# Optimization experiments

Measured on AMD Instinct MI355X. Metric: run time of the kernel, lower is better.

Reference implementation:

```python
import jax, jax.numpy as jnp
import numpy as np

N = 16      # hparams.length (utterances)
T = 128     # tokens per utterance
D = 256     # local_feature_dim
DG = 256    # global_attention.input_dim
ATT = 128   # attention inner dim
R1 = 2 * N * N  # rgcn num_relations
H1 = 256    # rgcn.dim
H2 = 256    # gcn.dim
NEG = -1e9


def setup_inputs() -> dict:
    ks = jax.random.split(jax.random.key(0), 16)
    s = 0.02
    return {
        "global_features": jax.random.normal(ks[0], (N, DG), jnp.float32),
        "local_features": jax.random.normal(ks[1], (N, T, D), jnp.float32),
        "speaker": jax.random.randint(ks[2], (N,), 0, 2),
        "length": jax.random.randint(ks[3], (N,), 1, T + 1),
        # Bahdanau global attention params
        "Wq": jax.random.normal(ks[4], (DG, ATT), jnp.float32) * s,
        "Wk": jax.random.normal(ks[5], (DG, ATT), jnp.float32) * s,
        "v_att": jax.random.normal(ks[6], (ATT,), jnp.float32) * s,
        # Bidirectional local attention params
        "Wb1": jax.random.normal(ks[7], (D, ATT), jnp.float32) * s,
        "Wb2": jax.random.normal(ks[8], (D, ATT), jnp.float32) * s,
        # RGCN layer 1 (2*N^2 relations)
        "Wrel1": jax.random.normal(ks[9], (R1, D, H1), jnp.float32) * s,
        "Wroot1": jax.random.normal(ks[10], (D, H1), jnp.float32) * s,
        "b1": jnp.zeros((H1,), jnp.float32),
        # RGCN layer 2 (1 relation)
        "Wrel2": jax.random.normal(ks[11], (1, H1, H2), jnp.float32) * s,
        "Wroot2": jax.random.normal(ks[12], (H1, H2), jnp.float32) * s,
        "b2": jnp.zeros((H2,), jnp.float32),
    }


def _rgcn_fg(x, Wrel, Wroot, b, e_src, e_dst, rel, ew, n_nodes):
    # x: [N,T,din], ew: [E,Ts,Td] (src-token x dst-token weights), Wrel: [R,din,dout]
    We = Wrel[rel]                 # [E,din,dout] irregular gather over relations
    xs = x[e_src]                  # [E,T,din]
    # message aligned with dst tokens: sum over src tokens t -> dst token s
    msg = jnp.einsum('ets,etd,edo->eso', ew, xs, We)   # [E,T,dout]
    agg = jax.ops.segment_sum(msg, e_dst, num_segments=n_nodes)
    return agg + x @ Wroot + b


def reference(global_features, local_features, speaker, length,
              Wq, Wk, v_att, Wb1, Wb2,
              Wrel1, Wroot1, b1, Wrel2, Wroot2, b2):
    n = global_features.shape[0]
    t = local_features.shape[1]

    # --- Bahdanau global attention: query i over keys j ---
    q = global_features @ Wq                         # [N,A]
    k = global_features @ Wk                         # [N,A]
    s = jnp.tanh(q[:, None, :] + k[None, :, :]) @ v_att   # [N,N]
    gw = jax.nn.softmax(s, axis=1).reshape(-1)       # [N*N]

    # --- Bidirectional local attention, vectorized over all (i,j) pairs ---
    p1 = local_features @ Wb1                        # [N,T,A]
    p2 = local_features @ Wb2                        # [N,T,A]
    S = jnp.einsum('ita,jsa->ijts', p1, p2)          # [N,N,T,T]
    pos = jnp.arange(t)
    valid = pos[None, :] < length[:, None]           # [N,T]
    S = jnp.where(valid[None, :, None, :], S, NEG)   # mask key tokens of j
    w1 = jax.nn.softmax(S, axis=-1)                  # softmax over j's tokens
    w1 = w1 * valid[:, None, :, None]                # zero padded query rows of i
    lw = w1.reshape(n * n, t, t)                     # [E,T,T]

    # --- edge weights & relation ids ---
    ew1 = gw[:, None, None] * lw                     # [E,T,T]
    e_src = jnp.arange(n * n) // n                   # edge (i,j): src=i
    e_dst = jnp.arange(n * n) % n                    # dst=j
    direction = jnp.where(e_src < e_dst, 0, 1)
    rel = (speaker[e_src] * n + speaker[e_dst]) * 2 + direction

    # --- two attention-weighted relational GCN layers ---
    x1 = _rgcn_fg(local_features, Wrel1, Wroot1, b1, e_src, e_dst, rel, ew1, n)
    x2 = _rgcn_fg(x1, Wrel2, Wroot2, b2, e_src, e_dst, jnp.zeros_like(rel), lw, n)
    return x2
```

## Files before the change

### kernel.cpp

```cpp
#include <hip/hip_runtime.h>

#define NODES 16
#define TT    128
#define DIM   256
#define ATTD  128
#define HD    256
#define NEGV  -1e9f

typedef short bf16x8 __attribute__((ext_vector_type(8)));
typedef float f32x4  __attribute__((ext_vector_type(4)));
typedef unsigned short ushort_t;
typedef ushort_t u16x4 __attribute__((ext_vector_type(4)));
typedef ushort_t u16x8 __attribute__((ext_vector_type(8)));

__device__ __forceinline__ ushort_t f2b(float f) {
  union { float f; unsigned u; } v; v.f = f;
  unsigned r = (v.u + 0x7fffu + ((v.u >> 16) & 1u)) >> 16;
  return (ushort_t)r;
}

__device__ __forceinline__ void wave_gemm_step(const ushort_t* __restrict__ A, int as, int R0,
                                               const ushort_t* __restrict__ BT, int bs, int C0,
                                               int kb, int lr, f32x4 acc[4][4]) {
  bf16x8 a[4], b[4];
#pragma unroll
  for (int m = 0; m < 4; ++m)
    a[m] = *(const bf16x8*)(A + (size_t)(R0 + m * 16 + lr) * as + kb);
#pragma unroll
  for (int n = 0; n < 4; ++n)
    b[n] = *(const bf16x8*)(BT + (size_t)(C0 + n * 16 + lr) * bs + kb);
#pragma unroll
  for (int m = 0; m < 4; ++m)
#pragma unroll
    for (int n = 0; n < 4; ++n)
      acc[m][n] = __builtin_amdgcn_mfma_f32_16x16x32_bf16(a[m], b[n], acc[m][n], 0, 0, 0);
}

#define WAVE_SETUP                                    \
  int tid = threadIdx.x;                              \
  int wave = tid >> 6, lane = tid & 63;               \
  int wr = wave >> 1, wc = wave & 1;                  \
  int lr = lane & 15, kg = lane >> 4;                 \
  (void)wr; (void)wc;

#define ACC_INIT(acc)                                 \
  f32x4 acc[4][4];                                    \
  { f32x4 z = {0.f, 0.f, 0.f, 0.f};                   \
    _Pragma("unroll") for (int m = 0; m < 4; ++m)     \
    _Pragma("unroll") for (int n = 0; n < 4; ++n) acc[m][n] = z; }

__device__ __forceinline__ void stage_tile(const ushort_t* __restrict__ src,
                                           ushort_t* __restrict__ dst, int tid) {
#pragma unroll
  for (int p = 0; p < 8; ++p) {
    int idx = p * 256 + tid;
    int row = idx >> 4;
    int cb  = (idx & 15) << 4;
    u16x8 v = *(const u16x8*)(src + (size_t)row * 128 + (cb >> 1));
    *(u16x8*)((char*)dst + row * 256 + (cb ^ ((row & 7) << 4))) = v;
  }
}

__device__ __forceinline__ void lds_gemm128(const ushort_t* __restrict__ A,
                                            const ushort_t* __restrict__ B,
                                            int R0, int C0, int lr, int kg,
                                            f32x4 acc[4][4]) {
#pragma unroll
  for (int kk = 0; kk < 4; ++kk) {
    int cb = kk * 64 + kg * 16;
    bf16x8 a[4], b[4];
#pragma unroll
    for (int m = 0; m < 4; ++m) {
      int row = R0 + m * 16 + lr;
      a[m] = *(const bf16x8*)((const char*)A + row * 256 + (cb ^ ((row & 7) << 4)));
    }
#pragma unroll
    for (int n = 0; n < 4; ++n) {
      int row = C0 + n * 16 + lr;
      b[n] = *(const bf16x8*)((const char*)B + row * 256 + (cb ^ ((row & 7) << 4)));
    }
#pragma unroll
    for (int m = 0; m < 4; ++m)
#pragma unroll
      for (int n = 0; n < 4; ++n)
        acc[m][n] = __builtin_amdgcn_mfma_f32_16x16x32_bf16(a[m], b[n], acc[m][n], 0, 0, 0);
  }
}

__global__ void k_prep(const float* __restrict__ Lf, ushort_t* __restrict__ Lfh,
                       const float* __restrict__ Wb1, const float* __restrict__ Wb2,
                       const float* __restrict__ Wroot1, const float* __restrict__ Wroot2,
                       const float* __restrict__ Wrel2, const float* __restrict__ Wrel1,
                       ushort_t* __restrict__ Wb1T, ushort_t* __restrict__ Wb2T,
                       ushort_t* __restrict__ Wroot1T, ushort_t* __restrict__ Wroot2T,
                       ushort_t* __restrict__ Wrel2T, ushort_t* __restrict__ Wrel1T8,
                       const float* __restrict__ G, const float* __restrict__ Wq,
                       const float* __restrict__ Wk, float* __restrict__ qk) {
  int blk = blockIdx.x;
  if (blk < 256) {
    int gi = blk * 256 + threadIdx.x;
    const float4* src = (const float4*)Lf;
    float4 v0 = src[gi * 2], v1 = src[gi * 2 + 1];
    u16x8 o;
    o[0] = f2b(v0.x); o[1] = f2b(v0.y); o[2] = f2b(v0.z); o[3] = f2b(v0.w);
    o[4] = f2b(v1.x); o[5] = f2b(v1.y); o[6] = f2b(v1.z); o[7] = f2b(v1.w);
    *(u16x8*)(Lfh + (size_t)gi * 8) = o;
  } else if (blk < 448) {
    __shared__ float lds[64][65];
    int b = blk - 256;
    const float* src; ushort_t* dst; int R, C, t;
    if (b < 8)       { src = Wb1;    dst = Wb1T;    R = 256; C = 128; t = b; }
    else if (b < 16) { src = Wb2;    dst = Wb2T;    R = 256; C = 128; t = b - 8; }
    else if (b < 32) { src = Wroot1; dst = Wroot1T; R = 256; C = 256; t = b - 16; }
    else if (b < 48) { src = Wroot2; dst = Wroot2T; R = 256; C = 256; t = b - 32; }
    else if (b < 64) { src = Wrel2;  dst = Wrel2T;  R = 256; C = 256; t = b - 48; }
    else {
      int m = (b - 64) >> 4;
      int relid = (m >> 2) * 32 + (m & 3);
      src = Wrel1 + (size_t)relid * 65536;
      dst = Wrel1T8 + (size_t)m * 65536;
      R = 256; C = 256; t = (b - 64) & 15;
    }
    int tilesC = C >> 6;
    int r0 = (t / tilesC) * 64, c0 = (t % tilesC) * 64;
    int tid = threadIdx.x;
    for (int p = 0; p < 16; ++p) {
      int idx = p * 256 + tid, rr = idx >> 6, cc = idx & 63;
      lds[rr][cc] = src[(size_t)(r0 + rr) * C + c0 + cc];
    }
    __syncthreads();
    for (int p = 0; p < 16; ++p) {
      int idx = p * 256 + tid, rr = idx >> 6, cc = idx & 63;
      dst[(size_t)(c0 + rr) * R + r0 + cc] = f2b(lds[cc][rr]);
    }
  } else {
    int i = blk - 448, t = threadIdx.x;
    const float* W = (t < 128) ? Wq : Wk;
    int a = t & 127;
    float acc = 0.f;
#pragma unroll 8
    for (int d = 0; d < DIM; ++d)
      acc = fmaf(G[i * DIM + d], W[d * ATTD + a], acc);
    int dst = (t < 128) ? i : (NODES + i);
    qk[(size_t)dst * ATTD + a] = acc;
  }
}

__global__ __launch_bounds__(256, 1)
void k_phaseB(const float* __restrict__ qk, const float* __restrict__ vatt,
              float* __restrict__ gw,
              const ushort_t* __restrict__ Lfh,
              const ushort_t* __restrict__ Wb1T, const ushort_t* __restrict__ Wb2T,
              ushort_t* __restrict__ p1h, ushort_t* __restrict__ p2h,
              const ushort_t* __restrict__ Wroot1T, const float* __restrict__ b1,
              float* __restrict__ x1part,
              const ushort_t* __restrict__ Wrel1T8, const int* __restrict__ spk,
              ushort_t* __restrict__ YT) {
  int blk = blockIdx.x;
  if (blk < 16) {
    __shared__ float sred[NODES][17];
    __shared__ float q[ATTD];
    int i = blk, t = threadIdx.x;
    int j = t >> 4, ag = t & 15;
    if (t < ATTD) q[t] = qk[(size_t)i * ATTD + t];
    __syncthreads();
    float sum = 0.f;
#pragma unroll
    for (int u = 0; u < 8; ++u) {
      int a = ag * 8 + u;
      sum += tanhf(q[a] + qk[(size_t)(NODES + j) * ATTD + a]) * vatt[a];
    }
    sred[j][ag] = sum;
    __syncthreads();
    if (t < NODES) {
      float s = 0.f;
#pragma unroll
      for (int u = 0; u < 16; ++u) s += sred[t][u];
      sred[t][16] = s;
    }
    __syncthreads();
    if (t == 0) {
      float m = -1e30f;
      for (int jj = 0; jj < NODES; ++jj) m = fmaxf(m, sred[jj][16]);
      float ex[NODES], ssum = 0.f;
      for (int jj = 0; jj < NODES; ++jj) { ex[jj] = __expf(sred[jj][16] - m); ssum += ex[jj]; }
      float inv = 1.f / ssum;
      for (int jj = 0; jj < NODES; ++jj) gw[i * NODES + jj] = ex[jj] * inv;
    }
  } else if (blk < 48) {
    int t = blk - 16;
    int sel = t >> 4, bx = t & 15;
    const ushort_t* BT = sel ? Wb2T : Wb1T;
    ushort_t* out = sel ? p2h : p1h;
    WAVE_SETUP
    int R0 = bx * 128 + wr * 64, C0 = wc * 64;
    ACC_INIT(acc)
    for (int kk = 0; kk < 8; ++kk)
      wave_gemm_step(Lfh, DIM, R0, BT, DIM, C0, kk * 32 + kg * 8, lr, acc);
#pragma unroll
    for (int m = 0; m < 4; ++m)
#pragma unroll
      for (int n = 0; n < 4; ++n) {
        int col = C0 + n * 16 + lr;
#pragma unroll
        for (int r = 0; r < 4; ++r) {
          int row = R0 + m * 16 + kg * 4 + r;
          out[(size_t)row * ATTD + col] = f2b(acc[m][n][r]);
        }
      }
  } else if (blk < 80) {
    int t = blk - 48;
    int bx = t & 15, by = t >> 4;
    WAVE_SETUP
    int R0 = bx * 128 + wr * 64, C0 = by * 128 + wc * 64;
    ACC_INIT(acc)
    for (int kk = 0; kk < 8; ++kk)
      wave_gemm_step(Lfh, DIM, R0, Wroot1T, DIM, C0, kk * 32 + kg * 8, lr, acc);
#pragma unroll
    for (int m = 0; m < 4; ++m)
#pragma unroll
      for (int n = 0; n < 4; ++n) {
        int col = C0 + n * 16 + lr;
        float bb = b1[col];
#pragma unroll
        for (int r = 0; r < 4; ++r) {
          int row = R0 + m * 16 + kg * 4 + r;
          x1part[(size_t)row * HD + col] = acc[m][n][r] + bb;
        }
      }
  } else {
    int t = blk - 80;
    int iq = t >> 1, cy = t & 1;
    int i = iq >> 2, q = iq & 3;
    int m8 = spk[i] * 4 + q;
    const ushort_t* A  = Lfh + (size_t)i * TT * DIM;
    const ushort_t* BT = Wrel1T8 + (size_t)m8 * 65536;
    WAVE_SETUP
    int R0 = wr * 64, C0 = cy * 128 + wc * 64;
    ACC_INIT(acc)
    for (int kk = 0; kk < 8; ++kk)
      wave_gemm_step(A, DIM, R0, BT, DIM, C0, kk * 32 + kg * 8, lr, acc);
#pragma unroll
    for (int m = 0; m < 4; ++m)
#pragma unroll
      for (int n = 0; n < 4; ++n) {
        int o = C0 + n * 16 + lr;
        int t0 = R0 + m * 16 + kg * 4;
        u16x4 v;
#pragma unroll
        for (int r = 0; r < 4; ++r) v[r] = f2b(acc[m][n][r]);
        *(u16x4*)(YT + (size_t)iq * 32768 + (size_t)o * TT + t0) = v;
      }
  }
}

__global__ __launch_bounds__(256, 1)
void k_locatt(const ushort_t* __restrict__ p1h, const ushort_t* __restrict__ p2h,
              const int* __restrict__ length,
              ushort_t* __restrict__ lwT) {
  __shared__ float S[TT][129];
  __shared__ float red[TT][2];
  __shared__ float sInv[TT];
  int e = blockIdx.x, i = e >> 4, j = e & 15;
  WAVE_SETUP
  int R0 = wr * 64, C0 = wc * 64;
  const ushort_t* A = p1h + (size_t)i * TT * ATTD;
  const ushort_t* B = p2h + (size_t)j * TT * ATTD;
  ACC_INIT(acc)
  for (int kk = 0; kk < 4; ++kk)
    wave_gemm_step(A, ATTD, R0, B, ATTD, C0, kk * 32 + kg * 8, lr, acc);
#pragma unroll
  for (int m = 0; m < 4; ++m)
#pragma unroll
    for (int n = 0; n < 4; ++n)
#pragma unroll
      for (int r = 0; r < 4; ++r)
        S[R0 + m * 16 + kg * 4 + r][C0 + n * 16 + lr] = acc[m][n][r];
  __syncthreads();
  int leni = length[i], lenj = length[j];
  int t = tid & 127, h = tid >> 7, s0 = h * 64;
  float mx = -1e30f;
  for (int s = s0; s < s0 + 64; ++s) {
    float vv = (s < lenj) ? S[t][s] : NEGV;
    mx = fmaxf(mx, vv);
  }
  red[t][h] = mx;
  __syncthreads();
  mx = fmaxf(red[t][0], red[t][1]);
  __syncthreads();
  float sum = 0.f;
  for (int s = s0; s < s0 + 64; ++s) {
    float vv = (s < lenj) ? S[t][s] : NEGV;
    float ee = __expf(vv - mx);
    S[t][s] = ee;
    sum += ee;
  }
  red[t][h] = sum;
  __syncthreads();
  if (h == 0) sInv[t] = (t < leni) ? 1.f / (red[t][0] + red[t][1]) : 0.f;
  __syncthreads();
  int s = tid >> 1;
  int t0 = (tid & 1) * 64;
  size_t base = (size_t)e * 16384 + (size_t)s * TT;
  for (int tb = 0; tb < 64; tb += 8) {
    u16x8 w;
#pragma unroll
    for (int u = 0; u < 8; ++u) {
      int tt = t0 + tb + u;
      w[u] = f2b(S[tt][s] * sInv[tt]);
    }
    *(u16x8*)(lwT + base + t0 + tb) = w;
  }
}

__global__ __launch_bounds__(256, 1)
void k_wagg(const ushort_t* __restrict__ lwT, const ushort_t* __restrict__ Bsrc,
            const float* __restrict__ gw, const int* __restrict__ spk,
            float* __restrict__ part, int mode) {
  __shared__ ushort_t lds[4][16384];
  int g = blockIdx.x, j = blockIdx.y, oh = blockIdx.z;
  WAVE_SETUP
  int R0 = wr * 64, C0 = wc * 64;
  int i0 = g * 2, i1 = g * 2 + 1;
  int e0 = i0 * NODES + j, e1 = i1 * NODES + j;
  const ushort_t* B0;
  const ushort_t* B1;
  float ge0, ge1;
  if (mode == 1) {
    int q0 = spk[j] * 2 + ((i0 < j) ? 0 : 1);
    int q1 = spk[j] * 2 + ((i1 < j) ? 0 : 1);
    B0 = Bsrc + (size_t)(i0 * 4 + q0) * 32768 + (size_t)oh * 16384;
    B1 = Bsrc + (size_t)(i1 * 4 + q1) * 32768 + (size_t)oh * 16384;
    ge0 = gw[e0]; ge1 = gw[e1];
  } else {
    B0 = Bsrc + (size_t)i0 * 32768 + (size_t)oh * 16384;
    B1 = Bsrc + (size_t)i1 * 32768 + (size_t)oh * 16384;
    ge0 = 1.f; ge1 = 1.f;
  }
  stage_tile(lwT + (size_t)e0 * 16384, lds[0], tid);
  stage_tile(B0, lds[1], tid);
  __syncthreads();
  stage_tile(lwT + (size_t)e1 * 16384, lds[2], tid);
  stage_tile(B1, lds[3], tid);
  ACC_INIT(acc0)
  lds_gemm128(lds[0], lds[1], R0, C0, lr, kg, acc0);
  __syncthreads();
  ACC_INIT(acc1)
  lds_gemm128(lds[2], lds[3], R0, C0, lr, kg, acc1);
  size_t base = (size_t)(g * NODES + j) * TT * HD + (size_t)oh * 128;
#pragma unroll
  for (int m = 0; m < 4; ++m)
#pragma unroll
    for (int n = 0; n < 4; ++n) {
      int ocol = C0 + n * 16 + lr;
#pragma unroll
      for (int r = 0; r < 4; ++r) {
        int s = R0 + m * 16 + kg * 4 + r;
        part[base + (size_t)s * HD + ocol] = ge0 * acc0[m][n][r] + ge1 * acc1[m][n][r];
      }
    }
}

__global__ __launch_bounds__(256, 1)
void k_reduce1(const float* __restrict__ part, const float* __restrict__ x1part,
               ushort_t* __restrict__ x1h, ushort_t* __restrict__ x1T) {
  __shared__ ushort_t L[TT][136];
  int j = blockIdx.x, oh = blockIdx.y, tid = threadIdx.x;
  const size_t Q = (size_t)NODES * TT * HD;
  for (int p = 0; p < 16; ++p) {
    int idx = p * 256 + tid;
    int t = idx >> 5, o4 = (idx & 31) * 4;
    size_t goff = ((size_t)j * TT + t) * HD + (size_t)oh * 128 + o4;
    float4 s = *(const float4*)(x1part + goff);
    for (int g = 0; g < 8; ++g) {
      float4 pv = *(const float4*)(part + (size_t)g * Q + goff);
      s.x += pv.x; s.y += pv.y; s.z += pv.z; s.w += pv.w;
    }
    u16x4 hv; hv[0] = f2b(s.x); hv[1] = f2b(s.y); hv[2] = f2b(s.z); hv[3] = f2b(s.w);
    *(u16x4*)(x1h + goff) = hv;
    *(u16x4*)(&L[t][o4]) = hv;
  }
  __syncthreads();
  for (int p = 0; p < 16; ++p) {
    int idx = p * 256 + tid;
    int o = idx >> 5, t4 = (idx & 31) * 4;
    u16x4 v;
#pragma unroll
    for (int u = 0; u < 4; ++u) v[u] = L[t4 + u][o];
    *(u16x4*)(x1T + (size_t)j * 32768 + (size_t)(oh * 128 + o) * TT + t4) = v;
  }
}

__global__ void k_reduce2(const float* __restrict__ part, ushort_t* __restrict__ Z2h) {
  int idx = blockIdx.x * 256 + threadIdx.x;
  size_t o4 = (size_t)idx * 4;
  const size_t Q = (size_t)NODES * TT * HD;
  float4 s = *(const float4*)(part + o4);
  for (int g = 1; g < 8; ++g) {
    float4 pv = *(const float4*)(part + (size_t)g * Q + o4);
    s.x += pv.x; s.y += pv.y; s.z += pv.z; s.w += pv.w;
  }
  u16x4 hv; hv[0] = f2b(s.x); hv[1] = f2b(s.y); hv[2] = f2b(s.z); hv[3] = f2b(s.w);
  *(u16x4*)(Z2h + o4) = hv;
}

__global__ __launch_bounds__(64, 1)
void k_final(const ushort_t* __restrict__ Z2h, const ushort_t* __restrict__ Wrel2T,
             const ushort_t* __restrict__ x1h, const ushort_t* __restrict__ Wroot2T,
             const float* __restrict__ b2, float* __restrict__ out) {
  int lane = threadIdx.x;
  int lr = lane & 15, kg = lane >> 4;
  int R0 = blockIdx.x * 64, C0 = blockIdx.y * 64;
  ACC_INIT(acc)
  for (int kk = 0; kk < 8; ++kk)
    wave_gemm_step(Z2h, HD, R0, Wrel2T, HD, C0, kk * 32 + kg * 8, lr, acc);
  for (int kk = 0; kk < 8; ++kk)
    wave_gemm_step(x1h, HD, R0, Wroot2T, HD, C0, kk * 32 + kg * 8, lr, acc);
#pragma unroll
  for (int m = 0; m < 4; ++m)
#pragma unroll
    for (int n = 0; n < 4; ++n) {
      int col = C0 + n * 16 + lr;
      float bb = b2[col];
#pragma unroll
      for (int r = 0; r < 4; ++r) {
        int row = R0 + m * 16 + kg * 4 + r;
        out[(size_t)row * HD + col] = acc[m][n][r] + bb;
      }
    }
}

extern "C" void kernel_launch(void* const* d_in, const int* in_sizes, int n_in,
                              void* d_out, int out_size, void* d_ws, size_t ws_size,
                              hipStream_t stream) {
  (void)in_sizes; (void)n_in; (void)out_size; (void)ws_size;
  const float* G      = (const float*)d_in[0];
  const float* Lf     = (const float*)d_in[1];
  const int*   spk    = (const int*)d_in[2];
  const int*   len    = (const int*)d_in[3];
  const float* Wq     = (const float*)d_in[4];
  const float* Wk     = (const float*)d_in[5];
  const float* vatt   = (const float*)d_in[6];
  const float* Wb1    = (const float*)d_in[7];
  const float* Wb2    = (const float*)d_in[8];
  const float* Wrel1  = (const float*)d_in[9];
  const float* Wroot1 = (const float*)d_in[10];
  const float* b1     = (const float*)d_in[11];
  const float* Wrel2  = (const float*)d_in[12];
  const float* Wroot2 = (const float*)d_in[13];
  const float* b2     = (const float*)d_in[14];

  char* ws = (char*)d_ws;
  const size_t MB = 1ull << 20;
  float*    gw      = (float*)(ws);
  float*    qk      = (float*)(ws + 16 * 1024);
  ushort_t* Lfh     = (ushort_t*)(ws + 1 * MB);
  ushort_t* Wb1T    = (ushort_t*)(ws + 2 * MB);
  ushort_t* Wb2T    = (ushort_t*)(ws + 2 * MB + 64 * 1024);
  ushort_t* Wroot1T = (ushort_t*)(ws + 2 * MB + 128 * 1024);
  ushort_t* Wroot2T = (ushort_t*)(ws + 2 * MB + 256 * 1024);
  ushort_t* Wrel2T  = (ushort_t*)(ws + 2 * MB + 384 * 1024);
  ushort_t* Wrel1T8 = (ushort_t*)(ws + 2 * MB + 512 * 1024);
  ushort_t* p1h     = (ushort_t*)(ws + 4 * MB);
  ushort_t* p2h     = (ushort_t*)(ws + 4 * MB + 512 * 1024);
  ushort_t* lwT     = (ushort_t*)(ws + 5 * MB);
  ushort_t* YT      = (ushort_t*)(ws + 21 * MB);
  float*    x1part  = (float*)(ws + 25 * MB);
  float*    part    = (float*)(ws + 27 * MB);
  ushort_t* x1h     = (ushort_t*)(ws + 43 * MB);
  ushort_t* x1T     = (ushort_t*)(ws + 44 * MB);
  ushort_t* Z2h     = (ushort_t*)(ws + 45 * MB);
  float* out = (float*)d_out;

  k_prep<<<464, 256, 0, stream>>>(Lf, Lfh, Wb1, Wb2, Wroot1, Wroot2, Wrel2, Wrel1,
                                  Wb1T, Wb2T, Wroot1T, Wroot2T, Wrel2T, Wrel1T8,
                                  G, Wq, Wk, qk);
  k_phaseB<<<208, 256, 0, stream>>>(qk, vatt, gw, Lfh, Wb1T, Wb2T, p1h, p2h,
                                    Wroot1T, b1, x1part, Wrel1T8, spk, YT);
  k_locatt<<<256, 256, 0, stream>>>(p1h, p2h, len, lwT);
  k_wagg<<<dim3(8, 16, 2), 256, 0, stream>>>(lwT, YT, gw, spk, part, 1);
  k_reduce1<<<dim3(16, 2), 256, 0, stream>>>(part, x1part, x1h, x1T);
  k_wagg<<<dim3(8, 16, 2), 256, 0, stream>>>(lwT, x1T, gw, spk, part, 2);
  k_reduce2<<<512, 256, 0, stream>>>(part, Z2h);
  k_final<<<dim3(32, 4), 64, 0, stream>>>(Z2h, Wrel2T, x1h, Wroot2T, b2, out);
}
```

Baseline: 91.29 us.

## Stage GEMM operands through swizzled LDS and widen reduce1 grid

Generalizes the LDS tile staging and GEMM helpers to a templated row width. The phase-B projection GEMMs and the local-attention score GEMM now stage A and B tiles into XOR-swizzled shared memory instead of loading MFMA fragments straight from global memory. Separately, k_reduce1 is split into 32-column slices across 128 blocks instead of 32, which adds parallelism to the partial-sum reduction and transpose. The cost is a large static LDS allocation in k_phaseB (128 KB) and k_locatt, which may limit occupancy. Every staging pass also waits on a barrier before any compute starts.

```diff
diff --git a/kernel.cpp b/kernel.cpp
--- a/kernel.cpp
+++ b/kernel.cpp
@@ -49,35 +49,39 @@
     _Pragma("unroll") for (int m = 0; m < 4; ++m)     \
     _Pragma("unroll") for (int n = 0; n < 4; ++n) acc[m][n] = z; }
 
-__device__ __forceinline__ void stage_tile(const ushort_t* __restrict__ src,
-                                           ushort_t* __restrict__ dst, int tid) {
-#pragma unroll
-  for (int p = 0; p < 8; ++p) {
+template <int ROWB>
+__device__ __forceinline__ void stage_tileN(const ushort_t* __restrict__ src,
+                                            ushort_t* __restrict__ dst, int tid) {
+  constexpr int CPR = ROWB / 16;
+  constexpr int PASSES = 128 * CPR / 256;
+#pragma unroll
+  for (int p = 0; p < PASSES; ++p) {
     int idx = p * 256 + tid;
-    int row = idx >> 4;
-    int cb  = (idx & 15) << 4;
-    u16x8 v = *(const u16x8*)(src + (size_t)row * 128 + (cb >> 1));
-    *(u16x8*)((char*)dst + row * 256 + (cb ^ ((row & 7) << 4))) = v;
-  }
-}
-
-__device__ __forceinline__ void lds_gemm128(const ushort_t* __restrict__ A,
-                                            const ushort_t* __restrict__ B,
-                                            int R0, int C0, int lr, int kg,
-                                            f32x4 acc[4][4]) {
-#pragma unroll
-  for (int kk = 0; kk < 4; ++kk) {
+    int row = idx / CPR;
+    int cb  = (idx % CPR) << 4;
+    u16x8 v = *(const u16x8*)(src + (size_t)row * (ROWB / 2) + (cb >> 1));
+    *(u16x8*)((char*)dst + row * ROWB + (cb ^ ((row & 7) << 4))) = v;
+  }
+}
+
+template <int ROWB>
+__device__ __forceinline__ void lds_gemmN(const ushort_t* __restrict__ A,
+                                          const ushort_t* __restrict__ B,
+                                          int R0, int C0, int lr, int kg,
+                                          f32x4 acc[4][4]) {
+#pragma unroll
+  for (int kk = 0; kk < ROWB / 64; ++kk) {
     int cb = kk * 64 + kg * 16;
     bf16x8 a[4], b[4];
 #pragma unroll
     for (int m = 0; m < 4; ++m) {
       int row = R0 + m * 16 + lr;
-      a[m] = *(const bf16x8*)((const char*)A + row * 256 + (cb ^ ((row & 7) << 4)));
+      a[m] = *(const bf16x8*)((const char*)A + row * ROWB + (cb ^ ((row & 7) << 4)));
     }
 #pragma unroll
     for (int n = 0; n < 4; ++n) {
       int row = C0 + n * 16 + lr;
-      b[n] = *(const bf16x8*)((const char*)B + row * 256 + (cb ^ ((row & 7) << 4)));
+      b[n] = *(const bf16x8*)((const char*)B + row * ROWB + (cb ^ ((row & 7) << 4)));
     }
 #pragma unroll
     for (int m = 0; m < 4; ++m)
@@ -156,6 +160,8 @@
               float* __restrict__ x1part,
               const ushort_t* __restrict__ Wrel1T8, const int* __restrict__ spk,
               ushort_t* __restrict__ YT) {
+  __shared__ ushort_t sA[32768];
+  __shared__ ushort_t sB[32768];
   int blk = blockIdx.x;
   if (blk < 16) {
     __shared__ float sred[NODES][17];
@@ -193,10 +199,12 @@
     const ushort_t* BT = sel ? Wb2T : Wb1T;
     ushort_t* out = sel ? p2h : p1h;
     WAVE_SETUP
+    stage_tileN<512>(Lfh + (size_t)bx * 128 * DIM, sA, tid);
+    stage_tileN<512>(BT, sB, tid);
+    __syncthreads();
+    ACC_INIT(acc)
+    lds_gemmN<512>(sA, sB, wr * 64, wc * 64, lr, kg, acc);
     int R0 = bx * 128 + wr * 64, C0 = wc * 64;
-    ACC_INIT(acc)
-    for (int kk = 0; kk < 8; ++kk)
-      wave_gemm_step(Lfh, DIM, R0, BT, DIM, C0, kk * 32 + kg * 8, lr, acc);
 #pragma unroll
     for (int m = 0; m < 4; ++m)
 #pragma unroll
@@ -212,10 +220,12 @@
     int t = blk - 48;
     int bx = t & 15, by = t >> 4;
     WAVE_SETUP
+    stage_tileN<512>(Lfh + (size_t)bx * 128 * DIM, sA, tid);
+    stage_tileN<512>(Wroot1T + (size_t)by * 128 * DIM, sB, tid);
+    __syncthreads();
+    ACC_INIT(acc)
+    lds_gemmN<512>(sA, sB, wr * 64, wc * 64, lr, kg, acc);
     int R0 = bx * 128 + wr * 64, C0 = by * 128 + wc * 64;
-    ACC_INIT(acc)
-    for (int kk = 0; kk < 8; ++kk)
-      wave_gemm_step(Lfh, DIM, R0, Wroot1T, DIM, C0, kk * 32 + kg * 8, lr, acc);
 #pragma unroll
     for (int m = 0; m < 4; ++m)
 #pragma unroll
@@ -233,13 +243,13 @@
     int iq = t >> 1, cy = t & 1;
     int i = iq >> 2, q = iq & 3;
     int m8 = spk[i] * 4 + q;
-    const ushort_t* A  = Lfh + (size_t)i * TT * DIM;
-    const ushort_t* BT = Wrel1T8 + (size_t)m8 * 65536;
     WAVE_SETUP
+    stage_tileN<512>(Lfh + (size_t)i * TT * DIM, sA, tid);
+    stage_tileN<512>(Wrel1T8 + (size_t)m8 * 65536 + (size_t)cy * 128 * DIM, sB, tid);
+    __syncthreads();
+    ACC_INIT(acc)
+    lds_gemmN<512>(sA, sB, wr * 64, wc * 64, lr, kg, acc);
     int R0 = wr * 64, C0 = cy * 128 + wc * 64;
-    ACC_INIT(acc)
-    for (int kk = 0; kk < 8; ++kk)
-      wave_gemm_step(A, DIM, R0, BT, DIM, C0, kk * 32 + kg * 8, lr, acc);
 #pragma unroll
     for (int m = 0; m < 4; ++m)
 #pragma unroll
@@ -258,17 +268,19 @@
 void k_locatt(const ushort_t* __restrict__ p1h, const ushort_t* __restrict__ p2h,
               const int* __restrict__ length,
               ushort_t* __restrict__ lwT) {
+  __shared__ ushort_t sA[16384];
+  __shared__ ushort_t sB[16384];
   __shared__ float S[TT][129];
   __shared__ float red[TT][2];
   __shared__ float sInv[TT];
   int e = blockIdx.x, i = e >> 4, j = e & 15;
   WAVE_SETUP
   int R0 = wr * 64, C0 = wc * 64;
-  const ushort_t* A = p1h + (size_t)i * TT * ATTD;
-  const ushort_t* B = p2h + (size_t)j * TT * ATTD;
+  stage_tileN<256>(p1h + (size_t)i * TT * ATTD, sA, tid);
+  stage_tileN<256>(p2h + (size_t)j * TT * ATTD, sB, tid);
+  __syncthreads();
   ACC_INIT(acc)
-  for (int kk = 0; kk < 4; ++kk)
-    wave_gemm_step(A, ATTD, R0, B, ATTD, C0, kk * 32 + kg * 8, lr, acc);
+  lds_gemmN<256>(sA, sB, R0, C0, lr, kg, acc);
 #pragma unroll
   for (int m = 0; m < 4; ++m)
 #pragma unroll
@@ -337,16 +349,16 @@
     B1 = Bsrc + (size_t)i1 * 32768 + (size_t)oh * 16384;
     ge0 = 1.f; ge1 = 1.f;
   }
-  stage_tile(lwT + (size_t)e0 * 16384, lds[0], tid);
-  stage_tile(B0, lds[1], tid);
-  __syncthreads();
-  stage_tile(lwT + (size_t)e1 * 16384, lds[2], tid);
-  stage_tile(B1, lds[3], tid);
+  stage_tileN<256>(lwT + (size_t)e0 * 16384, lds[0], tid);
+  stage_tileN<256>(B0, lds[1], tid);
+  __syncthreads();
+  stage_tileN<256>(lwT + (size_t)e1 * 16384, lds[2], tid);
+  stage_tileN<256>(B1, lds[3], tid);
   ACC_INIT(acc0)
-  lds_gemm128(lds[0], lds[1], R0, C0, lr, kg, acc0);
+  lds_gemmN<256>(lds[0], lds[1], R0, C0, lr, kg, acc0);
   __syncthreads();
   ACC_INIT(acc1)
-  lds_gemm128(lds[2], lds[3], R0, C0, lr, kg, acc1);
+  lds_gemmN<256>(lds[2], lds[3], R0, C0, lr, kg, acc1);
   size_t base = (size_t)(g * NODES + j) * TT * HD + (size_t)oh * 128;
 #pragma unroll
   for (int m = 0; m < 4; ++m)
@@ -364,14 +376,16 @@
 __global__ __launch_bounds__(256, 1)
 void k_reduce1(const float* __restrict__ part, const float* __restrict__ x1part,
                ushort_t* __restrict__ x1h, ushort_t* __restrict__ x1T) {
-  __shared__ ushort_t L[TT][136];
-  int j = blockIdx.x, oh = blockIdx.y, tid = threadIdx.x;
+  __shared__ ushort_t L[TT][40];
+  int j = blockIdx.x, oc0 = blockIdx.y * 32, tid = threadIdx.x;
   const size_t Q = (size_t)NODES * TT * HD;
-  for (int p = 0; p < 16; ++p) {
+#pragma unroll
+  for (int p = 0; p < 4; ++p) {
     int idx = p * 256 + tid;
-    int t = idx >> 5, o4 = (idx & 31) * 4;
-    size_t goff = ((size_t)j * TT + t) * HD + (size_t)oh * 128 + o4;
+    int t = idx >> 3, o4 = (idx & 7) * 4;
+    size_t goff = ((size_t)j * TT + t) * HD + oc0 + o4;
     float4 s = *(const float4*)(x1part + goff);
+#pragma unroll
     for (int g = 0; g < 8; ++g) {
       float4 pv = *(const float4*)(part + (size_t)g * Q + goff);
       s.x += pv.x; s.y += pv.y; s.z += pv.z; s.w += pv.w;
@@ -381,13 +395,14 @@
     *(u16x4*)(&L[t][o4]) = hv;
   }
   __syncthreads();
-  for (int p = 0; p < 16; ++p) {
+#pragma unroll
+  for (int p = 0; p < 2; ++p) {
     int idx = p * 256 + tid;
-    int o = idx >> 5, t4 = (idx & 31) * 4;
-    u16x4 v;
-#pragma unroll
-    for (int u = 0; u < 4; ++u) v[u] = L[t4 + u][o];
-    *(u16x4*)(x1T + (size_t)j * 32768 + (size_t)(oh * 128 + o) * TT + t4) = v;
+    int o = idx >> 4, t8 = (idx & 15) * 8;
+    u16x8 v;
+#pragma unroll
+    for (int u = 0; u < 8; ++u) v[u] = L[t8 + u][o];
+    *(u16x8*)(x1T + (size_t)j * 32768 + (size_t)(oc0 + o) * TT + t8) = v;
   }
 }
 
@@ -479,7 +494,7 @@
                                     Wroot1T, b1, x1part, Wrel1T8, spk, YT);
   k_locatt<<<256, 256, 0, stream>>>(p1h, p2h, len, lwT);
   k_wagg<<<dim3(8, 16, 2), 256, 0, stream>>>(lwT, YT, gw, spk, part, 1);
-  k_reduce1<<<dim3(16, 2), 256, 0, stream>>>(part, x1part, x1h, x1T);
+  k_reduce1<<<dim3(16, 8), 256, 0, stream>>>(part, x1part, x1h, x1T);
   k_wagg<<<dim3(8, 16, 2), 256, 0, stream>>>(lwT, x1T, gw, spk, part, 2);
   k_reduce2<<<512, 256, 0, stream>>>(part, Z2h);
   k_final<<<dim3(32, 4), 64, 0, stream>>>(Z2h, Wrel2T, x1h, Wroot2T, b2, out);
```

Result: faster. 77.57 us (-15.0%).
